# Kernel tuning notes

Hardware: AMD Instinct MI355X
Metric: run time of the kernel (lower is better)

Reference implementation:

```python
import jax, jax.numpy as jnp
import numpy as np

HIDDEN_DIM = 512


def setup_inputs() -> dict:
    key = jax.random.key(0)
    ks = jax.random.split(key, 7)
    B, SQ, SKV, DIN, H = 8, 2048, 2048, 1024, HIDDEN_DIM
    query = jax.random.normal(ks[0], (B, SQ, H), dtype=jnp.float32)
    states = jax.random.normal(ks[1], (B, SKV, DIN), dtype=jnp.float32)
    mask = jax.random.uniform(ks[2], (B, SQ, SKV), dtype=jnp.float32)
    # LazyLinear params (stored as [in, out]; torch uses x @ W.T with W [out, in])
    Wk = jax.random.normal(ks[3], (DIN, H), dtype=jnp.float32) * (1.0 / np.sqrt(DIN))
    bk = jax.random.normal(ks[4], (H,), dtype=jnp.float32) * 0.02
    Wv = jax.random.normal(ks[5], (DIN, H), dtype=jnp.float32) * (1.0 / np.sqrt(DIN))
    bv = jax.random.normal(ks[6], (H,), dtype=jnp.float32) * 0.02
    return {"query": query, "states": states, "mask": mask,
            "Wk": Wk, "bk": bk, "Wv": Wv, "bv": bv}


def reference(query, states, mask, Wk, bk, Wv, bv):
    # transform_states=True: project states into key/value spaces
    keys = states @ Wk + bk        # [B, S_kv, H]
    values = states @ Wv + bv      # [B, S_kv, H]
    # bmm(query, keys^T) / sqrt(H)
    scale = 1.0 / jnp.sqrt(jnp.asarray(keys.shape[-1], dtype=query.dtype))
    scores = jnp.einsum('bqh,bkh->bqk', query, keys) * scale  # [B, S_q, S_kv]
    scores = mask * scores  # multiplicative mask
    # source detaches the softmax output
    attn = jax.lax.stop_gradient(jax.nn.softmax(scores, axis=-1))
    return jnp.einsum('bqk,bkh->bqh', attn, values)  # [B, S_q, H]
```

## Files before the change

kernel.cpp:

```cpp
#include <hip/hip_runtime.h>
#include <hip/hip_bf16.h>
#include <stdint.h>

#define BM 128
#define BN 128
#define BK 32

typedef __bf16 bf16;
typedef bf16 bf16x4 __attribute__((ext_vector_type(4)));
typedef bf16 bf16x8 __attribute__((ext_vector_type(8)));
typedef float f32x4 __attribute__((ext_vector_type(4)));

typedef const __attribute__((address_space(1))) void* gas1_t;
typedef __attribute__((address_space(3))) void* las3_t;

__device__ __forceinline__ void gl_lds16(const void* g, void* l) {
  __builtin_amdgcn_global_load_lds((gas1_t)g, (las3_t)l, 16, 0, 0);
}

__device__ __forceinline__ void gemm_core(const bf16* A, const bf16* Bt,
                                          int lda, int ldb, int kTiles,
                                          bf16* As, bf16* Bs, f32x4 acc[4][4]) {
  const int tid = threadIdx.x;
  const int lane = tid & 63;
  const int wid = tid >> 6;
  const int wr = wid >> 1, wc = wid & 1;
  const int lr = lane & 15, lg = lane >> 4;

  for (int kt = 0; kt < kTiles; ++kt) {
    const bf16* Ak = A + kt * BK;
    const bf16* Bk = Bt + kt * BK;
#pragma unroll
    for (int p = 0; p < 2; ++p) {
      int c = p * 256 + tid;
      int row = c >> 2, k8 = (c & 3) << 3;
      gl_lds16(Ak + (size_t)row * lda + k8, As + c * 8);
      gl_lds16(Bk + (size_t)row * ldb + k8, Bs + c * 8);
    }
    __syncthreads();
    bf16x8 af[4], bfr[4];
#pragma unroll
    for (int i = 0; i < 4; ++i) {
      af[i]  = *(const bf16x8*)(As + (wr * 64 + i * 16 + lr) * BK + lg * 8);
      bfr[i] = *(const bf16x8*)(Bs + (wc * 64 + i * 16 + lr) * BK + lg * 8);
    }
#pragma unroll
    for (int i = 0; i < 4; ++i)
#pragma unroll
      for (int j = 0; j < 4; ++j)
        acc[i][j] = __builtin_amdgcn_mfma_f32_16x16x32_bf16(af[i], bfr[j], acc[i][j], 0, 0, 0);
    __syncthreads();
  }
}

__global__ __launch_bounds__(256) void k_cast(const float* __restrict__ in,
                                              bf16* __restrict__ out, int n8) {
  int i = blockIdx.x * blockDim.x + threadIdx.x;
  int stride = gridDim.x * blockDim.x;
  for (; i < n8; i += stride) {
    float4 a = ((const float4*)in)[2 * (size_t)i];
    float4 b = ((const float4*)in)[2 * (size_t)i + 1];
    bf16x8 o;
    o[0] = (bf16)a.x; o[1] = (bf16)a.y; o[2] = (bf16)a.z; o[3] = (bf16)a.w;
    o[4] = (bf16)b.x; o[5] = (bf16)b.y; o[6] = (bf16)b.z; o[7] = (bf16)b.w;
    ((bf16x8*)out)[i] = o;
  }
}

__global__ __launch_bounds__(256) void k_transposeW(const float* __restrict__ Wk,
                                                    const float* __restrict__ Wv,
                                                    bf16* __restrict__ WT) {
  __shared__ float t[32][33];
  const float* W = blockIdx.z ? Wv : Wk;
  bf16* O = WT + (size_t)blockIdx.z * 512 * 1024;
  int h0 = blockIdx.x * 32, d0 = blockIdx.y * 32;
  int tx = threadIdx.x & 31, ty = threadIdx.x >> 5;
#pragma unroll
  for (int yy = 0; yy < 4; ++yy)
    t[ty + yy * 8][tx] = W[(size_t)(d0 + ty + yy * 8) * 512 + h0 + tx];
  __syncthreads();
#pragma unroll
  for (int yy = 0; yy < 4; ++yy)
    O[(size_t)(h0 + ty + yy * 8) * 1024 + d0 + tx] = (bf16)t[tx][ty + yy * 8];
}

__global__ __launch_bounds__(256) void k_projK(const bf16* __restrict__ WkT,
                                               const bf16* __restrict__ S,
                                               const float* __restrict__ bk,
                                               bf16* __restrict__ Kb) {
  __shared__ bf16 As[BM * BK], Bs[BN * BK];
  f32x4 acc[4][4] = {};
  int h0 = blockIdx.x * BM, t0 = blockIdx.y * BN;
  gemm_core(WkT + (size_t)h0 * 1024, S + (size_t)t0 * 1024, 1024, 1024, 1024 / BK, As, Bs, acc);
  const int lane = threadIdx.x & 63, wid = threadIdx.x >> 6;
  const int wr = wid >> 1, wc = wid & 1, lr = lane & 15, lg = lane >> 4;
#pragma unroll
  for (int i = 0; i < 4; ++i) {
    int hb = h0 + wr * 64 + i * 16 + lg * 4;
    float4 bias = *(const float4*)(bk + hb);
#pragma unroll
    for (int j = 0; j < 4; ++j) {
      int t = t0 + wc * 64 + j * 16 + lr;
      f32x4 v = acc[i][j];
      bf16x4 o;
      o[0] = (bf16)(v[0] + bias.x); o[1] = (bf16)(v[1] + bias.y);
      o[2] = (bf16)(v[2] + bias.z); o[3] = (bf16)(v[3] + bias.w);
      *(bf16x4*)(Kb + (size_t)t * 512 + hb) = o;
    }
  }
}

__global__ __launch_bounds__(256) void k_projV(const bf16* __restrict__ S,
                                               const bf16* __restrict__ WvT,
                                               const float* __restrict__ bv,
                                               bf16* __restrict__ VT) {
  __shared__ bf16 As[BM * BK], Bs[BN * BK];
  f32x4 acc[4][4] = {};
  int t0 = blockIdx.x * BM, h0 = blockIdx.y * BN;
  gemm_core(S + (size_t)t0 * 1024, WvT + (size_t)h0 * 1024, 1024, 1024, 1024 / BK, As, Bs, acc);
  const int lane = threadIdx.x & 63, wid = threadIdx.x >> 6;
  const int wr = wid >> 1, wc = wid & 1, lr = lane & 15, lg = lane >> 4;
#pragma unroll
  for (int i = 0; i < 4; ++i) {
    int tb = t0 + wr * 64 + i * 16 + lg * 4;
    int b = tb >> 11, s = tb & 2047;
#pragma unroll
    for (int j = 0; j < 4; ++j) {
      int h = h0 + wc * 64 + j * 16 + lr;
      float bias = bv[h];
      f32x4 v = acc[i][j];
      bf16x4 o;
      o[0] = (bf16)(v[0] + bias); o[1] = (bf16)(v[1] + bias);
      o[2] = (bf16)(v[2] + bias); o[3] = (bf16)(v[3] + bias);
      *(bf16x4*)(VT + ((size_t)(b * 512 + h)) * 2048 + s) = o;
    }
  }
}

__global__ __launch_bounds__(256) void k_scores(const bf16* __restrict__ Kb,
                                                const bf16* __restrict__ Qb,
                                                const float* __restrict__ mask,
                                                bf16* __restrict__ P,
                                                float* __restrict__ lsum) {
  __shared__ bf16 As[BM * BK], Bs[BN * BK];
  f32x4 acc[4][4] = {};
  int b = blockIdx.z;
  int kv0 = blockIdx.x * BM, q0 = blockIdx.y * BN;
  gemm_core(Kb + (size_t)b * 2048 * 512 + (size_t)kv0 * 512,
            Qb + (size_t)b * 2048 * 512 + (size_t)q0 * 512, 512, 512, 512 / BK, As, Bs, acc);
  const float scale = 0.04419417382415922f;
  const float* Mb = mask + (size_t)b * 2048 * 2048;
  bf16* Pb = P + (size_t)b * 2048 * 2048;
  const int lane = threadIdx.x & 63, wid = threadIdx.x >> 6;
  const int wr = wid >> 1, wc = wid & 1, lr = lane & 15, lg = lane >> 4;
  float rs[4] = {0.f, 0.f, 0.f, 0.f};
#pragma unroll
  for (int j = 0; j < 4; ++j) {
    int q = q0 + wc * 64 + j * 16 + lr;
    size_t qrow = (size_t)q * 2048;
#pragma unroll
    for (int i = 0; i < 4; ++i) {
      int kvb = kv0 + wr * 64 + i * 16 + lg * 4;
      float4 m4 = *(const float4*)(Mb + qrow + kvb);
      f32x4 v = acc[i][j];
      float p0 = __expf(v[0] * scale * m4.x);
      float p1 = __expf(v[1] * scale * m4.y);
      float p2 = __expf(v[2] * scale * m4.z);
      float p3 = __expf(v[3] * scale * m4.w);
      bf16x4 o; o[0] = (bf16)p0; o[1] = (bf16)p1; o[2] = (bf16)p2; o[3] = (bf16)p3;
      *(bf16x4*)(Pb + qrow + kvb) = o;
      rs[j] += p0 + p1 + p2 + p3;
    }
  }
#pragma unroll
  for (int j = 0; j < 4; ++j) {
    float v = rs[j];
    v += __shfl_xor(v, 16);
    v += __shfl_xor(v, 32);
    if (lane < 16)
      atomicAdd(&lsum[b * 2048 + q0 + wc * 64 + j * 16 + lr], v);
  }
}

__global__ __launch_bounds__(256) void k_pv(const bf16* __restrict__ VT,
                                            const bf16* __restrict__ P,
                                            const float* __restrict__ lsum,
                                            float* __restrict__ out) {
  __shared__ bf16 As[BM * BK], Bs[BN * BK];
  f32x4 acc[4][4] = {};
  int b = blockIdx.z;
  int h0 = blockIdx.x * BM, q0 = blockIdx.y * BN;
  gemm_core(VT + (size_t)b * 512 * 2048 + (size_t)h0 * 2048,
            P + (size_t)b * 2048 * 2048 + (size_t)q0 * 2048, 2048, 2048, 2048 / BK, As, Bs, acc);
  float* Ob = out + (size_t)b * 2048 * 512;
  const float* lb = lsum + b * 2048;
  const int lane = threadIdx.x & 63, wid = threadIdx.x >> 6;
  const int wr = wid >> 1, wc = wid & 1, lr = lane & 15, lg = lane >> 4;
#pragma unroll
  for (int j = 0; j < 4; ++j) {
    int q = q0 + wc * 64 + j * 16 + lr;
    float inv = 1.0f / lb[q];
#pragma unroll
    for (int i = 0; i < 4; ++i) {
      int hb = h0 + wr * 64 + i * 16 + lg * 4;
      f32x4 v = acc[i][j];
      float4 o4 = make_float4(v[0] * inv, v[1] * inv, v[2] * inv, v[3] * inv);
      *(float4*)(Ob + (size_t)q * 512 + hb) = o4;
    }
  }
}

extern "C" void kernel_launch(void* const* d_in, const int* in_sizes, int n_in,
                              void* d_out, int out_size, void* d_ws, size_t ws_size,
                              hipStream_t stream) {
  const float* query  = (const float*)d_in[0];
  const float* states = (const float*)d_in[1];
  const float* mask   = (const float*)d_in[2];
  const float* Wk     = (const float*)d_in[3];
  const float* bk     = (const float*)d_in[4];
  const float* Wv     = (const float*)d_in[5];
  const float* bv     = (const float*)d_in[6];
  float* out = (float*)d_out;

  char* ws = (char*)d_ws;
  bf16* WT = (bf16*)(ws);
  bf16* Qb = (bf16*)(ws + (2ull << 20));
  bf16* Kb = (bf16*)(ws + (18ull << 20));
  bf16* VT = (bf16*)(ws + (34ull << 20));
  bf16* Sb = (bf16*)(ws + (50ull << 20));
  bf16* P  = (bf16*)(ws + (50ull << 20));
  float* ls = (float*)(ws + (114ull << 20));

  bf16* WkT = WT;
  bf16* WvT = WT + (size_t)512 * 1024;

  hipMemsetAsync(ls, 0, 8 * 2048 * sizeof(float), stream);
  k_transposeW<<<dim3(16, 32, 2), 256, 0, stream>>>(Wk, Wv, WT);
  k_cast<<<dim3(2048), 256, 0, stream>>>(states, Sb, 16384 * 1024 / 8);
  k_cast<<<dim3(1024), 256, 0, stream>>>(query, Qb, 8 * 2048 * 512 / 8);
  k_projK<<<dim3(4, 128), 256, 0, stream>>>(WkT, Sb, bk, Kb);
  k_projV<<<dim3(128, 4), 256, 0, stream>>>(Sb, WvT, bv, VT);
  k_scores<<<dim3(16, 16, 8), 256, 0, stream>>>(Kb, Qb, mask, P, ls);
  k_pv<<<dim3(4, 16, 8), 256, 0, stream>>>(VT, P, ls, out);
}
```

Measured before the change: 450.1 us.

## Merge cast and projection launches, prefetch mask during scores GEMM loop

The two cast kernels become one launch over both tensors, and the K and V projections become one launch split on blockIdx.z, which removes launch gaps and tail underutilisation. In the scores kernel the GEMM loop is inlined and each k-tile iteration also issues one float4 mask load into registers, so mask latency overlaps the MFMA work instead of being paid in the epilogue. Holding 16 float4 mask values raises register pressure and may reduce occupancy.

Result: no change. 451.8 us (+0.4%).

```diff
diff --git a/kernel.cpp b/kernel.cpp
--- a/kernel.cpp
+++ b/kernel.cpp
@@ -53,17 +53,23 @@
   }
 }
 
-__global__ __launch_bounds__(256) void k_cast(const float* __restrict__ in,
-                                              bf16* __restrict__ out, int n8) {
+__global__ __launch_bounds__(256) void k_cast2(const float* __restrict__ a,
+                                               bf16* __restrict__ oa, int na8,
+                                               const float* __restrict__ b,
+                                               bf16* __restrict__ ob, int nb8) {
   int i = blockIdx.x * blockDim.x + threadIdx.x;
   int stride = gridDim.x * blockDim.x;
-  for (; i < n8; i += stride) {
-    float4 a = ((const float4*)in)[2 * (size_t)i];
-    float4 b = ((const float4*)in)[2 * (size_t)i + 1];
+  int ntot = na8 + nb8;
+  for (; i < ntot; i += stride) {
+    const float* src = (i < na8) ? a : b;
+    bf16* dst = (i < na8) ? oa : ob;
+    int idx = (i < na8) ? i : i - na8;
+    float4 x = ((const float4*)src)[2 * (size_t)idx];
+    float4 y = ((const float4*)src)[2 * (size_t)idx + 1];
     bf16x8 o;
-    o[0] = (bf16)a.x; o[1] = (bf16)a.y; o[2] = (bf16)a.z; o[3] = (bf16)a.w;
-    o[4] = (bf16)b.x; o[5] = (bf16)b.y; o[6] = (bf16)b.z; o[7] = (bf16)b.w;
-    ((bf16x8*)out)[i] = o;
+    o[0] = (bf16)x.x; o[1] = (bf16)x.y; o[2] = (bf16)x.z; o[3] = (bf16)x.w;
+    o[4] = (bf16)y.x; o[5] = (bf16)y.y; o[6] = (bf16)y.z; o[7] = (bf16)y.w;
+    ((bf16x8*)dst)[idx] = o;
   }
 }
 
@@ -84,55 +90,49 @@
     O[(size_t)(h0 + ty + yy * 8) * 1024 + d0 + tx] = (bf16)t[tx][ty + yy * 8];
 }
 
-__global__ __launch_bounds__(256) void k_projK(const bf16* __restrict__ WkT,
-                                               const bf16* __restrict__ S,
-                                               const float* __restrict__ bk,
-                                               bf16* __restrict__ Kb) {
+__global__ __launch_bounds__(256) void k_proj(const bf16* __restrict__ WT,
+                                              const bf16* __restrict__ S,
+                                              const float* __restrict__ bk,
+                                              const float* __restrict__ bv,
+                                              bf16* __restrict__ Kb,
+                                              bf16* __restrict__ VT) {
   __shared__ bf16 As[BM * BK], Bs[BN * BK];
   f32x4 acc[4][4] = {};
   int h0 = blockIdx.x * BM, t0 = blockIdx.y * BN;
-  gemm_core(WkT + (size_t)h0 * 1024, S + (size_t)t0 * 1024, 1024, 1024, 1024 / BK, As, Bs, acc);
   const int lane = threadIdx.x & 63, wid = threadIdx.x >> 6;
   const int wr = wid >> 1, wc = wid & 1, lr = lane & 15, lg = lane >> 4;
-#pragma unroll
-  for (int i = 0; i < 4; ++i) {
-    int hb = h0 + wr * 64 + i * 16 + lg * 4;
-    float4 bias = *(const float4*)(bk + hb);
-#pragma unroll
-    for (int j = 0; j < 4; ++j) {
-      int t = t0 + wc * 64 + j * 16 + lr;
-      f32x4 v = acc[i][j];
-      bf16x4 o;
-      o[0] = (bf16)(v[0] + bias.x); o[1] = (bf16)(v[1] + bias.y);
-      o[2] = (bf16)(v[2] + bias.z); o[3] = (bf16)(v[3] + bias.w);
-      *(bf16x4*)(Kb + (size_t)t * 512 + hb) = o;
-    }
-  }
-}
-
-__global__ __launch_bounds__(256) void k_projV(const bf16* __restrict__ S,
-                                               const bf16* __restrict__ WvT,
-                                               const float* __restrict__ bv,
-                                               bf16* __restrict__ VT) {
-  __shared__ bf16 As[BM * BK], Bs[BN * BK];
-  f32x4 acc[4][4] = {};
-  int t0 = blockIdx.x * BM, h0 = blockIdx.y * BN;
-  gemm_core(S + (size_t)t0 * 1024, WvT + (size_t)h0 * 1024, 1024, 1024, 1024 / BK, As, Bs, acc);
-  const int lane = threadIdx.x & 63, wid = threadIdx.x >> 6;
-  const int wr = wid >> 1, wc = wid & 1, lr = lane & 15, lg = lane >> 4;
-#pragma unroll
-  for (int i = 0; i < 4; ++i) {
-    int tb = t0 + wr * 64 + i * 16 + lg * 4;
-    int b = tb >> 11, s = tb & 2047;
-#pragma unroll
-    for (int j = 0; j < 4; ++j) {
-      int h = h0 + wc * 64 + j * 16 + lr;
-      float bias = bv[h];
-      f32x4 v = acc[i][j];
-      bf16x4 o;
-      o[0] = (bf16)(v[0] + bias); o[1] = (bf16)(v[1] + bias);
-      o[2] = (bf16)(v[2] + bias); o[3] = (bf16)(v[3] + bias);
-      *(bf16x4*)(VT + ((size_t)(b * 512 + h)) * 2048 + s) = o;
+  if (blockIdx.z == 0) {
+    gemm_core(WT + (size_t)h0 * 1024, S + (size_t)t0 * 1024, 1024, 1024, 1024 / BK, As, Bs, acc);
+#pragma unroll
+    for (int i = 0; i < 4; ++i) {
+      int hb = h0 + wr * 64 + i * 16 + lg * 4;
+      float4 bias = *(const float4*)(bk + hb);
+#pragma unroll
+      for (int j = 0; j < 4; ++j) {
+        int t = t0 + wc * 64 + j * 16 + lr;
+        f32x4 v = acc[i][j];
+        bf16x4 o;
+        o[0] = (bf16)(v[0] + bias.x); o[1] = (bf16)(v[1] + bias.y);
+        o[2] = (bf16)(v[2] + bias.z); o[3] = (bf16)(v[3] + bias.w);
+        *(bf16x4*)(Kb + (size_t)t * 512 + hb) = o;
+      }
+    }
+  } else {
+    gemm_core(S + (size_t)t0 * 1024, WT + (size_t)(512 + h0) * 1024, 1024, 1024, 1024 / BK, As, Bs, acc);
+#pragma unroll
+    for (int i = 0; i < 4; ++i) {
+      int tb = t0 + wr * 64 + i * 16 + lg * 4;
+      int b = tb >> 11, s = tb & 2047;
+#pragma unroll
+      for (int j = 0; j < 4; ++j) {
+        int h = h0 + wc * 64 + j * 16 + lr;
+        float bias = bv[h];
+        f32x4 v = acc[i][j];
+        bf16x4 o;
+        o[0] = (bf16)(v[0] + bias); o[1] = (bf16)(v[1] + bias);
+        o[2] = (bf16)(v[2] + bias); o[3] = (bf16)(v[3] + bias);
+        *(bf16x4*)(VT + ((size_t)(b * 512 + h)) * 2048 + s) = o;
+      }
     }
   }
 }
@@ -144,15 +144,44 @@
                                                 float* __restrict__ lsum) {
   __shared__ bf16 As[BM * BK], Bs[BN * BK];
   f32x4 acc[4][4] = {};
-  int b = blockIdx.z;
-  int kv0 = blockIdx.x * BM, q0 = blockIdx.y * BN;
-  gemm_core(Kb + (size_t)b * 2048 * 512 + (size_t)kv0 * 512,
-            Qb + (size_t)b * 2048 * 512 + (size_t)q0 * 512, 512, 512, 512 / BK, As, Bs, acc);
+  float4 mreg[16];
+  const int b = blockIdx.z;
+  const int kv0 = blockIdx.x * BM, q0 = blockIdx.y * BN;
+  const bf16* A  = Kb + (size_t)b * 2048 * 512 + (size_t)kv0 * 512;
+  const bf16* Bt = Qb + (size_t)b * 2048 * 512 + (size_t)q0 * 512;
+  const float* Mb = mask + (size_t)b * 2048 * 2048;
+  const int tid = threadIdx.x, lane = tid & 63, wid = tid >> 6;
+  const int wr = wid >> 1, wc = wid & 1, lr = lane & 15, lg = lane >> 4;
+#pragma unroll
+  for (int kt = 0; kt < 16; ++kt) {
+#pragma unroll
+    for (int p = 0; p < 2; ++p) {
+      int c = p * 256 + tid;
+      int row = c >> 2, k8 = (c & 3) << 3;
+      gl_lds16(A + (size_t)row * 512 + kt * BK + k8, As + c * 8);
+      gl_lds16(Bt + (size_t)row * 512 + kt * BK + k8, Bs + c * 8);
+    }
+    {
+      int q = q0 + wc * 64 + (kt >> 2) * 16 + lr;
+      int kvb = kv0 + wr * 64 + (kt & 3) * 16 + lg * 4;
+      mreg[kt] = *(const float4*)(Mb + (size_t)q * 2048 + kvb);
+    }
+    __syncthreads();
+    bf16x8 af[4], bfr[4];
+#pragma unroll
+    for (int i = 0; i < 4; ++i) {
+      af[i]  = *(const bf16x8*)(As + (wr * 64 + i * 16 + lr) * BK + lg * 8);
+      bfr[i] = *(const bf16x8*)(Bs + (wc * 64 + i * 16 + lr) * BK + lg * 8);
+    }
+#pragma unroll
+    for (int i = 0; i < 4; ++i)
+#pragma unroll
+      for (int j = 0; j < 4; ++j)
+        acc[i][j] = __builtin_amdgcn_mfma_f32_16x16x32_bf16(af[i], bfr[j], acc[i][j], 0, 0, 0);
+    __syncthreads();
+  }
   const float scale = 0.04419417382415922f;
-  const float* Mb = mask + (size_t)b * 2048 * 2048;
   bf16* Pb = P + (size_t)b * 2048 * 2048;
-  const int lane = threadIdx.x & 63, wid = threadIdx.x >> 6;
-  const int wr = wid >> 1, wc = wid & 1, lr = lane & 15, lg = lane >> 4;
   float rs[4] = {0.f, 0.f, 0.f, 0.f};
 #pragma unroll
   for (int j = 0; j < 4; ++j) {
@@ -161,7 +190,7 @@
 #pragma unroll
     for (int i = 0; i < 4; ++i) {
       int kvb = kv0 + wr * 64 + i * 16 + lg * 4;
-      float4 m4 = *(const float4*)(Mb + qrow + kvb);
+      float4 m4 = mreg[j * 4 + i];
       f32x4 v = acc[i][j];
       float p0 = __expf(v[0] * scale * m4.x);
       float p1 = __expf(v[1] * scale * m4.y);
@@ -231,15 +260,11 @@
   bf16* P  = (bf16*)(ws + (50ull << 20));
   float* ls = (float*)(ws + (114ull << 20));
 
-  bf16* WkT = WT;
-  bf16* WvT = WT + (size_t)512 * 1024;
-
   hipMemsetAsync(ls, 0, 8 * 2048 * sizeof(float), stream);
   k_transposeW<<<dim3(16, 32, 2), 256, 0, stream>>>(Wk, Wv, WT);
-  k_cast<<<dim3(2048), 256, 0, stream>>>(states, Sb, 16384 * 1024 / 8);
-  k_cast<<<dim3(1024), 256, 0, stream>>>(query, Qb, 8 * 2048 * 512 / 8);
-  k_projK<<<dim3(4, 128), 256, 0, stream>>>(WkT, Sb, bk, Kb);
-  k_projV<<<dim3(128, 4), 256, 0, stream>>>(Sb, WvT, bv, VT);
+  k_cast2<<<dim3(3072), 256, 0, stream>>>(states, Sb, 16384 * 1024 / 8,
+                                          query, Qb, 8 * 2048 * 512 / 8);
+  k_proj<<<dim3(4, 128, 2), 256, 0, stream>>>(WT, Sb, bk, bv, Kb, VT);
   k_scores<<<dim3(16, 16, 8), 256, 0, stream>>>(Kb, Qb, mask, P, ls);
   k_pv<<<dim3(4, 16, 8), 256, 0, stream>>>(VT, P, ls, out);
 }
```
